# Optimization experiments

Hardware: AMD Instinct MI355X
Metric: run time of the kernel (lower is better)

## Reference

```python
import jax, jax.numpy as jnp
import numpy as np

IN_F = 1024
OUT_F = 1024
GRID = 8
TOKENS = 8192


def setup_inputs() -> dict:
    key = jax.random.key(0)
    k_x, k_w, k_b, k_s = jax.random.split(key, 4)
    x = jax.random.normal(k_x, (TOKENS, IN_F), dtype=jnp.float32)
    # kaiming_uniform_(nonlinearity='linear'): bound = sqrt(3/fan_in)
    bound_w = float(np.sqrt(3.0 / IN_F))
    W = jax.random.uniform(k_w, (OUT_F, IN_F), minval=-bound_w, maxval=bound_w, dtype=jnp.float32)
    # nn.Linear default bias init: U(-1/sqrt(fan_in), 1/sqrt(fan_in))
    bound_b = float(1.0 / np.sqrt(IN_F))
    b = jax.random.uniform(k_b, (OUT_F,), minval=-bound_b, maxval=bound_b, dtype=jnp.float32)
    spline_weight = jax.random.uniform(k_s, (OUT_F, IN_F, GRID), minval=-0.1, maxval=0.1, dtype=jnp.float32)
    grid = jnp.linspace(-3.0, 3.0, GRID, dtype=jnp.float32)
    return {"x": x, "W": W, "b": b, "spline_weight": spline_weight, "grid": grid}


def reference(x, W, b, spline_weight, grid):
    grid_size = spline_weight.shape[-1]
    # base path: Linear(silu(x))
    base = jnp.einsum('ti,oi->to', jax.nn.silu(x), W) + b
    # RBF basis: [tokens, in_features, grid_size]
    denom = 2.0 / (grid_size - 1) + 1e-05
    basis = jnp.exp(-(((x[..., None] - grid) / denom) ** 2))
    spline = jnp.einsum('tig,oig->to', basis, spline_weight)
    return base + spline
```

## Files before the change

kernel.cpp:

```cpp
#include <hip/hip_runtime.h>
#include <hip/hip_bf16.h>

#define IN_F   1024
#define OUT_F  1024
#define TOKENS 8192
#define KTOT   9216
#define KHALF  4608
#define NTILE  72

typedef __attribute__((ext_vector_type(8))) short  bf16x8;
typedef __attribute__((ext_vector_type(4))) float  f32x4;

template<int M> struct ModeT { static constexpr int value = M; };

__device__ __forceinline__ unsigned int f2bf(float f) {
    union { float f; unsigned int u; } v; v.f = f;
    unsigned int r = v.u + 0x7fffu + ((v.u >> 16) & 1u);
    return r >> 16;
}

__device__ __forceinline__ void prep_a_body(int idx, const float* __restrict__ x,
                                            const float* __restrict__ grid,
                                            unsigned short* __restrict__ A)
{
    int t = idx >> 10;
    int i = idx & 1023;
    float xv = x[idx];
    float sil = xv / (1.0f + __expf(-xv));
    A[(size_t)t * KTOT + i] = (unsigned short)f2bf(sil);

    const float invd = 1.0f / (2.0f / 7.0f + 1e-5f);
    unsigned int h[8];
    #pragma unroll
    for (int g = 0; g < 8; ++g) {
        float d = (xv - grid[g]) * invd;
        h[g] = f2bf(__expf(-d * d));
    }
    uint4 pk;
    pk.x = h[0] | (h[1] << 16);
    pk.y = h[2] | (h[3] << 16);
    pk.z = h[4] | (h[5] << 16);
    pk.w = h[6] | (h[7] << 16);
    *reinterpret_cast<uint4*>(&A[(size_t)t * KTOT + IN_F + (size_t)i * 8]) = pk;
}

__device__ __forceinline__ void prep_b_body(int idx, const float* __restrict__ W,
                                            const float* __restrict__ spl,
                                            unsigned short* __restrict__ B)
{
    int o  = idx / (KTOT / 8);
    int c8 = idx - o * (KTOT / 8);
    const float* src = (c8 < IN_F / 8)
        ? (W   + (size_t)o * IN_F     + (size_t)c8 * 8)
        : (spl + (size_t)o * IN_F * 8 + (size_t)(c8 - IN_F / 8) * 8);
    const float4* s4 = reinterpret_cast<const float4*>(src);
    float4 lo = s4[0], hi = s4[1];
    uint4 pk;
    pk.x = f2bf(lo.x) | (f2bf(lo.y) << 16);
    pk.y = f2bf(lo.z) | (f2bf(lo.w) << 16);
    pk.z = f2bf(hi.x) | (f2bf(hi.y) << 16);
    pk.w = f2bf(hi.z) | (f2bf(hi.w) << 16);
    *reinterpret_cast<uint4*>(&B[(size_t)o * KTOT + (size_t)c8 * 8]) = pk;
}

__global__ __launch_bounds__(256)
void prep_fused(const float* __restrict__ x, const float* __restrict__ grid,
                const float* __restrict__ W, const float* __restrict__ spl,
                unsigned short* __restrict__ A, unsigned short* __restrict__ B)
{
    int b = blockIdx.x;
    if (b < (TOKENS * IN_F) / 256)
        prep_a_body(b * 256 + threadIdx.x, x, grid, A);
    else
        prep_b_body((b - (TOKENS * IN_F) / 256) * 256 + threadIdx.x, W, spl, B);
}

__global__ __launch_bounds__(256)
void prep_a_kernel(const float* __restrict__ x, const float* __restrict__ grid,
                   unsigned short* __restrict__ A)
{
    prep_a_body(blockIdx.x * blockDim.x + threadIdx.x, x, grid, A);
}

__global__ __launch_bounds__(256)
void prep_b_kernel(const float* __restrict__ W, const float* __restrict__ spl,
                   unsigned short* __restrict__ B)
{
    prep_b_body(blockIdx.x * blockDim.x + threadIdx.x, W, spl, B);
}

#define GLOAD(src, dst) __builtin_amdgcn_global_load_lds( \
    (const __attribute__((address_space(1))) void*)(src),  \
    (__attribute__((address_space(3))) void*)(dst), 16, 0, 0)
#define SBAR()  __builtin_amdgcn_s_barrier()
#define SCH0()  __builtin_amdgcn_sched_barrier(0)
#define VMC0()  asm volatile("s_waitcnt vmcnt(0)" ::: "memory")

__global__ __launch_bounds__(512, 2)
void gemm_kan2(const unsigned short* __restrict__ A,
               const unsigned short* __restrict__ B,
               float* __restrict__ P, int rows)
{
    __shared__ char lds[131072];

    const int bid  = blockIdx.x;
    const int xcd  = bid & 7;
    const int j    = bid >> 3;
    const int sk   = j & 1;
    const int bn   = (j >> 1) & 3;
    const int bm   = (j >> 3) * 8 + xcd;
    const int tid  = threadIdx.x;
    const int wave = tid >> 6, lane = tid & 63;
    const int wr   = wave >> 2, wc = wave & 3;
    const int fr   = lane & 15, kg = lane >> 4;
    const int sw   = fr & 7;
    const int koff[2] = { (kg ^ sw) * 16, ((4 | kg) ^ sw) * 16 };
    const int k0 = sk * KHALF;

    const int trow = tid >> 3;
    const int ksrc = ((tid & 7) ^ (trow & 7)) * 8;
    const unsigned short* gA = A + (size_t)(bm * 256 + trow) * KTOT + k0 + ksrc;
    const unsigned short* gB = B + (size_t)(bn * 256 + trow) * KTOT + k0 + ksrc;
    const size_t R64 = (size_t)64 * KTOT;

    f32x4 acc[8][4];
    const f32x4 zero = {0.f, 0.f, 0.f, 0.f};
    #pragma unroll
    for (int m = 0; m < 8; ++m)
        #pragma unroll
        for (int n = 0; n < 4; ++n) acc[m][n] = zero;

    {
        char* dA = lds + tid * 16;
        char* dB = lds + 65536 + tid * 16;
        GLOAD(gA,           dA);           GLOAD(gA + R64,     dA + 8192);
        GLOAD(gA + 2 * R64, dA + 16384);   GLOAD(gA + 3 * R64, dA + 24576);
        GLOAD(gB,           dB);           GLOAD(gB + R64,     dB + 8192);
        GLOAD(gB + 2 * R64, dB + 16384);   GLOAD(gB + 3 * R64, dB + 24576);
        gA += 64; gB += 64;
    }
    VMC0(); SBAR(); SCH0();

    const int aOff = (wr * 64 + fr) * 128;
    const int bOff = (wc * 32 + fr) * 128;

    bf16x8 af[4][2], bfLo[2][2], bfHi[2][2];
    int u = 0;

    auto tile = [&](auto mC) {
        constexpr int MODE = decltype(mC)::value;
        char* bufA = lds + (u & 1) * 32768;
        char* bufB = lds + 65536 + (u & 1) * 32768;

        #pragma unroll
        for (int mi = 0; mi < 4; ++mi)
            #pragma unroll
            for (int ks = 0; ks < 2; ++ks)
                af[mi][ks] = *(const bf16x8*)(bufA + aOff + mi * 2048 + koff[ks]);
        #pragma unroll
        for (int ni = 0; ni < 2; ++ni)
            #pragma unroll
            for (int ks = 0; ks < 2; ++ks) {
                bfLo[ni][ks] = *(const bf16x8*)(bufB + bOff + ni * 2048 + koff[ks]);
                bfHi[ni][ks] = *(const bf16x8*)(bufB + bOff + 16384 + ni * 2048 + koff[ks]);
            }

        if constexpr (MODE == 0) {
            char* dA = lds + ((u & 1) ^ 1) * 32768 + tid * 16;
            char* dB = lds + 65536 + ((u & 1) ^ 1) * 32768 + tid * 16;
            GLOAD(gA,           dA);           GLOAD(gA + R64,     dA + 8192);
            GLOAD(gA + 2 * R64, dA + 16384);   GLOAD(gA + 3 * R64, dA + 24576);
            GLOAD(gB,           dB);           GLOAD(gB + R64,     dB + 8192);
            GLOAD(gB + 2 * R64, dB + 16384);   GLOAD(gB + 3 * R64, dB + 24576);
            gA += 64; gB += 64;
        }
        SCH0();

        __builtin_amdgcn_s_setprio(1);
        #pragma unroll
        for (int mi = 0; mi < 4; ++mi)
            #pragma unroll
            for (int ni = 0; ni < 2; ++ni)
                #pragma unroll
                for (int ks = 0; ks < 2; ++ks)
                    acc[mi][ni] = __builtin_amdgcn_mfma_f32_16x16x32_bf16(
                        af[mi][ks], bfLo[ni][ks], acc[mi][ni], 0, 0, 0);
        __builtin_amdgcn_s_setprio(0);

        __builtin_amdgcn_s_setprio(1);
        #pragma unroll
        for (int mi = 0; mi < 4; ++mi)
            #pragma unroll
            for (int ni = 0; ni < 2; ++ni)
                #pragma unroll
                for (int ks = 0; ks < 2; ++ks)
                    acc[mi][2 + ni] = __builtin_amdgcn_mfma_f32_16x16x32_bf16(
                        af[mi][ks], bfHi[ni][ks], acc[mi][2 + ni], 0, 0, 0);
        __builtin_amdgcn_s_setprio(0);

        #pragma unroll
        for (int mi = 0; mi < 4; ++mi)
            #pragma unroll
            for (int ks = 0; ks < 2; ++ks)
                af[mi][ks] = *(const bf16x8*)(bufA + aOff + 16384 + mi * 2048 + koff[ks]);

        __builtin_amdgcn_s_setprio(1);
        #pragma unroll
        for (int mi = 0; mi < 4; ++mi)
            #pragma unroll
            for (int ni = 0; ni < 2; ++ni)
                #pragma unroll
                for (int ks = 0; ks < 2; ++ks)
                    acc[4 + mi][ni] = __builtin_amdgcn_mfma_f32_16x16x32_bf16(
                        af[mi][ks], bfLo[ni][ks], acc[4 + mi][ni], 0, 0, 0);
        __builtin_amdgcn_s_setprio(0);

        __builtin_amdgcn_s_setprio(1);
        #pragma unroll
        for (int mi = 0; mi < 4; ++mi)
            #pragma unroll
            for (int ni = 0; ni < 2; ++ni)
                #pragma unroll
                for (int ks = 0; ks < 2; ++ks)
                    acc[4 + mi][2 + ni] = __builtin_amdgcn_mfma_f32_16x16x32_bf16(
                        af[mi][ks], bfHi[ni][ks], acc[4 + mi][2 + ni], 0, 0, 0);
        __builtin_amdgcn_s_setprio(0);

        SCH0();
        if constexpr (MODE == 0) {
            VMC0();
            SBAR(); SCH0();
        }
    };

    for (u = 0; u < NTILE - 1; ++u) tile(ModeT<0>{});
    tile(ModeT<1>{});

    float* Pp = P + (size_t)sk * rows * OUT_F;
    const size_t orow0 = (size_t)bm * 256 + (size_t)wr * 64;
    const int    ocol0 = bn * 256 + wc * 32;
    #pragma unroll
    for (int n = 0; n < 4; ++n) {
        const int col = ocol0 + (n & 1) * 16 + (n >> 1) * 128 + fr;
        #pragma unroll
        for (int m = 0; m < 8; ++m) {
            const size_t r0 = orow0 + (m & 3) * 16 + (m >> 2) * 128 + kg * 4;
            #pragma unroll
            for (int j2 = 0; j2 < 4; ++j2)
                Pp[(r0 + j2) * OUT_F + col] = acc[m][n][j2];
        }
    }
}

__global__ __launch_bounds__(256)
void reduce_kan(const float* __restrict__ P, const float* __restrict__ bias,
                float* __restrict__ out, int n4, int skStride4)
{
    const float4* p0 = (const float4*)P;
    const float4* p1 = p0 + skStride4;
    const float4* bv = (const float4*)bias;
    float4* o = (float4*)out;
    for (int i = blockIdx.x * blockDim.x + threadIdx.x; i < n4;
         i += gridDim.x * blockDim.x) {
        float4 a = p0[i], b = p1[i], c = bv[i & 255];
        float4 r;
        r.x = a.x + b.x + c.x;  r.y = a.y + b.y + c.y;
        r.z = a.z + b.z + c.z;  r.w = a.w + b.w + c.w;
        o[i] = r;
    }
}

extern "C" void kernel_launch(void* const* d_in, const int* in_sizes, int n_in,
                              void* d_out, int out_size, void* d_ws, size_t ws_size,
                              hipStream_t stream)
{
    const float* x    = (const float*)d_in[0];
    const float* W    = (const float*)d_in[1];
    const float* bias = (const float*)d_in[2];
    const float* spl  = (const float*)d_in[3];
    const float* grid = (const float*)d_in[4];
    float* out = (float*)d_out;

    unsigned short* Bw = (unsigned short*)d_ws;
    unsigned short* Aw = Bw + (size_t)OUT_F * KTOT;

    const size_t bBytes = (size_t)OUT_F * KTOT * 2;
    size_t avail = ws_size > bBytes ? ws_size - bBytes : 0;
    long maxRows = (long)(avail / 26624);
    int chunk = (maxRows >= TOKENS) ? TOKENS : (int)((maxRows / 256) * 256);
    if (chunk < 256) chunk = 256;
    float* Pp = (float*)(Aw + (size_t)chunk * KTOT);

    if (chunk == TOKENS) {
        prep_fused<<<(TOKENS * IN_F) / 256 + (OUT_F * (KTOT / 8)) / 256,
                     256, 0, stream>>>(x, grid, W, spl, Aw, Bw);
        gemm_kan2<<<(TOKENS >> 8) * 8, 512, 0, stream>>>(Aw, Bw, Pp, TOKENS);
        int n4 = TOKENS * 256;
        reduce_kan<<<2048, 256, 0, stream>>>(Pp, bias, out, n4, n4);
    } else {
        prep_b_kernel<<<(OUT_F * (KTOT / 8)) / 256, 256, 0, stream>>>(W, spl, Bw);
        for (int t0 = 0; t0 < TOKENS; t0 += chunk) {
            int rows = (TOKENS - t0 < chunk) ? (TOKENS - t0) : chunk;
            prep_a_kernel<<<(rows * IN_F) / 256, 256, 0, stream>>>(
                x + (size_t)t0 * IN_F, grid, Aw);
            gemm_kan2<<<(rows >> 8) * 8, 512, 0, stream>>>(Aw, Bw, Pp, rows);
            int n4 = rows * 256;
            int rblocks = (n4 + 255) / 256; if (rblocks > 2048) rblocks = 2048;
            reduce_kan<<<rblocks, 256, 0, stream>>>(
                Pp, bias, out + (size_t)t0 * OUT_F, n4, n4);
        }
    }
}
```

Before: 199.1 us.

## Load B fragments directly from global into registers, halve LDS usage

Drops the LDS staging of the B operand: each wave now reads its B fragments straight from global memory into registers and prefetches the next k-step mid-tile, so only A is double-buffered in LDS (64KB instead of 128KB). The A fragments for both halves are loaded up front and the MFMA order is rearranged around the B loads. The XCD-aware block swizzle is also removed in favour of a plain linear block mapping. This frees LDS and cuts LDS traffic, possibly allowing more resident blocks, but B reads lose cross-wave sharing, and the remaining cost is uncoalesced global reads with latency exposed at the per-tile vmcnt(0) wait.

```diff
diff --git a/kernel.cpp b/kernel.cpp
--- a/kernel.cpp
+++ b/kernel.cpp
@@ -101,14 +101,12 @@
                const unsigned short* __restrict__ B,
                float* __restrict__ P, int rows)
 {
-    __shared__ char lds[131072];
+    __shared__ char lds[65536];
 
     const int bid  = blockIdx.x;
-    const int xcd  = bid & 7;
-    const int j    = bid >> 3;
-    const int sk   = j & 1;
-    const int bn   = (j >> 1) & 3;
-    const int bm   = (j >> 3) * 8 + xcd;
+    const int sk   = bid & 1;
+    const int bn   = (bid >> 1) & 3;
+    const int bm   = bid >> 3;
     const int tid  = threadIdx.x;
     const int wave = tid >> 6, lane = tid & 63;
     const int wr   = wave >> 2, wc = wave & 3;
@@ -120,8 +118,12 @@
     const int trow = tid >> 3;
     const int ksrc = ((tid & 7) ^ (trow & 7)) * 8;
     const unsigned short* gA = A + (size_t)(bm * 256 + trow) * KTOT + k0 + ksrc;
-    const unsigned short* gB = B + (size_t)(bn * 256 + trow) * KTOT + k0 + ksrc;
     const size_t R64 = (size_t)64 * KTOT;
+
+    const unsigned short* gB00 = B + (size_t)(bn * 256 + wc * 32 + fr) * KTOT + k0 + kg * 8;
+    const unsigned short* gB01 = gB00 + (size_t)16  * KTOT;
+    const unsigned short* gB10 = gB00 + (size_t)128 * KTOT;
+    const unsigned short* gB11 = gB00 + (size_t)144 * KTOT;
 
     f32x4 acc[8][4];
     const f32x4 zero = {0.f, 0.f, 0.f, 0.f};
@@ -130,49 +132,48 @@
         #pragma unroll
         for (int n = 0; n < 4; ++n) acc[m][n] = zero;
 
+    bf16x8 afLo[4][2], afHi[4][2], bfL[2][2], bfH[2][2];
+
     {
         char* dA = lds + tid * 16;
-        char* dB = lds + 65536 + tid * 16;
         GLOAD(gA,           dA);           GLOAD(gA + R64,     dA + 8192);
         GLOAD(gA + 2 * R64, dA + 16384);   GLOAD(gA + 3 * R64, dA + 24576);
-        GLOAD(gB,           dB);           GLOAD(gB + R64,     dB + 8192);
-        GLOAD(gB + 2 * R64, dB + 16384);   GLOAD(gB + 3 * R64, dB + 24576);
-        gA += 64; gB += 64;
+        gA += 64;
+        #pragma unroll
+        for (int ks = 0; ks < 2; ++ks) {
+            bfL[0][ks] = *(const bf16x8*)(gB00 + ks * 32);
+            bfL[1][ks] = *(const bf16x8*)(gB01 + ks * 32);
+        }
     }
     VMC0(); SBAR(); SCH0();
 
     const int aOff = (wr * 64 + fr) * 128;
-    const int bOff = (wc * 32 + fr) * 128;
-
-    bf16x8 af[4][2], bfLo[2][2], bfHi[2][2];
+
     int u = 0;
 
     auto tile = [&](auto mC) {
         constexpr int MODE = decltype(mC)::value;
         char* bufA = lds + (u & 1) * 32768;
-        char* bufB = lds + 65536 + (u & 1) * 32768;
-
-        #pragma unroll
-        for (int mi = 0; mi < 4; ++mi)
-            #pragma unroll
-            for (int ks = 0; ks < 2; ++ks)
-                af[mi][ks] = *(const bf16x8*)(bufA + aOff + mi * 2048 + koff[ks]);
-        #pragma unroll
-        for (int ni = 0; ni < 2; ++ni)
+
+        #pragma unroll
+        for (int mi = 0; mi < 4; ++mi)
             #pragma unroll
             for (int ks = 0; ks < 2; ++ks) {
-                bfLo[ni][ks] = *(const bf16x8*)(bufB + bOff + ni * 2048 + koff[ks]);
-                bfHi[ni][ks] = *(const bf16x8*)(bufB + bOff + 16384 + ni * 2048 + koff[ks]);
+                afLo[mi][ks] = *(const bf16x8*)(bufA + aOff + mi * 2048 + koff[ks]);
+                afHi[mi][ks] = *(const bf16x8*)(bufA + aOff + 16384 + mi * 2048 + koff[ks]);
             }
+
+        #pragma unroll
+        for (int ks = 0; ks < 2; ++ks) {
+            bfH[0][ks] = *(const bf16x8*)(gB10 + ks * 32);
+            bfH[1][ks] = *(const bf16x8*)(gB11 + ks * 32);
+        }
 
         if constexpr (MODE == 0) {
             char* dA = lds + ((u & 1) ^ 1) * 32768 + tid * 16;
-            char* dB = lds + 65536 + ((u & 1) ^ 1) * 32768 + tid * 16;
             GLOAD(gA,           dA);           GLOAD(gA + R64,     dA + 8192);
             GLOAD(gA + 2 * R64, dA + 16384);   GLOAD(gA + 3 * R64, dA + 24576);
-            GLOAD(gB,           dB);           GLOAD(gB + R64,     dB + 8192);
-            GLOAD(gB + 2 * R64, dB + 16384);   GLOAD(gB + 3 * R64, dB + 24576);
-            gA += 64; gB += 64;
+            gA += 64;
         }
         SCH0();
 
@@ -184,8 +185,27 @@
                 #pragma unroll
                 for (int ks = 0; ks < 2; ++ks)
                     acc[mi][ni] = __builtin_amdgcn_mfma_f32_16x16x32_bf16(
-                        af[mi][ks], bfLo[ni][ks], acc[mi][ni], 0, 0, 0);
+                        afLo[mi][ks], bfL[ni][ks], acc[mi][ni], 0, 0, 0);
         __builtin_amdgcn_s_setprio(0);
+
+        __builtin_amdgcn_s_setprio(1);
+        #pragma unroll
+        for (int mi = 0; mi < 4; ++mi)
+            #pragma unroll
+            for (int ni = 0; ni < 2; ++ni)
+                #pragma unroll
+                for (int ks = 0; ks < 2; ++ks)
+                    acc[4 + mi][ni] = __builtin_amdgcn_mfma_f32_16x16x32_bf16(
+                        afHi[mi][ks], bfL[ni][ks], acc[4 + mi][ni], 0, 0, 0);
+        __builtin_amdgcn_s_setprio(0);
+
+        if constexpr (MODE == 0) {
+            #pragma unroll
+            for (int ks = 0; ks < 2; ++ks) {
+                bfL[0][ks] = *(const bf16x8*)(gB00 + 64 + ks * 32);
+                bfL[1][ks] = *(const bf16x8*)(gB01 + 64 + ks * 32);
+            }
+        }
 
         __builtin_amdgcn_s_setprio(1);
         #pragma unroll
@@ -195,24 +215,7 @@
                 #pragma unroll
                 for (int ks = 0; ks < 2; ++ks)
                     acc[mi][2 + ni] = __builtin_amdgcn_mfma_f32_16x16x32_bf16(
-                        af[mi][ks], bfHi[ni][ks], acc[mi][2 + ni], 0, 0, 0);
-        __builtin_amdgcn_s_setprio(0);
-
-        #pragma unroll
-        for (int mi = 0; mi < 4; ++mi)
-            #pragma unroll
-            for (int ks = 0; ks < 2; ++ks)
-                af[mi][ks] = *(const bf16x8*)(bufA + aOff + 16384 + mi * 2048 + koff[ks]);
-
-        __builtin_amdgcn_s_setprio(1);
-        #pragma unroll
-        for (int mi = 0; mi < 4; ++mi)
-            #pragma unroll
-            for (int ni = 0; ni < 2; ++ni)
-                #pragma unroll
-                for (int ks = 0; ks < 2; ++ks)
-                    acc[4 + mi][ni] = __builtin_amdgcn_mfma_f32_16x16x32_bf16(
-                        af[mi][ks], bfLo[ni][ks], acc[4 + mi][ni], 0, 0, 0);
+                        afLo[mi][ks], bfH[ni][ks], acc[mi][2 + ni], 0, 0, 0);
         __builtin_amdgcn_s_setprio(0);
 
         __builtin_amdgcn_s_setprio(1);
@@ -223,13 +226,14 @@
                 #pragma unroll
                 for (int ks = 0; ks < 2; ++ks)
                     acc[4 + mi][2 + ni] = __builtin_amdgcn_mfma_f32_16x16x32_bf16(
-                        af[mi][ks], bfHi[ni][ks], acc[4 + mi][2 + ni], 0, 0, 0);
+                        afHi[mi][ks], bfH[ni][ks], acc[4 + mi][2 + ni], 0, 0, 0);
         __builtin_amdgcn_s_setprio(0);
 
         SCH0();
         if constexpr (MODE == 0) {
             VMC0();
             SBAR(); SCH0();
+            gB00 += 64; gB01 += 64; gB10 += 64; gB11 += 64;
         }
     };
 
```

Measured after the change: 262.6 us. 1.32x slower.

## Deepen GEMM pipeline with two tiles in flight and register-level fragment prefetch

Applied to the files above, without the earlier changes.

Restructures the bf16 MFMA main loop so two K-tiles of global-to-LDS loads are in flight and the next half-tile's LDS fragments are loaded into registers while the current MFMAs run. A single barrier per tile now separates consumption from refill, and the loop is split into steady, penultimate and last phases. The block-index mapping also drops the XCD-aware swizzle in favour of a plain linear decode. This raises register pressure from the doubled fragment sets and may change L2 locality across XCDs.

```diff
diff --git a/kernel.cpp b/kernel.cpp
--- a/kernel.cpp
+++ b/kernel.cpp
@@ -94,7 +94,9 @@
     (__attribute__((address_space(3))) void*)(dst), 16, 0, 0)
 #define SBAR()  __builtin_amdgcn_s_barrier()
 #define SCH0()  __builtin_amdgcn_sched_barrier(0)
+#define LGKM0() asm volatile("s_waitcnt lgkmcnt(0)" ::: "memory")
 #define VMC0()  asm volatile("s_waitcnt vmcnt(0)" ::: "memory")
+#define VMCNT_(n) asm volatile("s_waitcnt vmcnt(" #n ")" ::: "memory")
 
 __global__ __launch_bounds__(512, 2)
 void gemm_kan2(const unsigned short* __restrict__ A,
@@ -104,17 +106,16 @@
     __shared__ char lds[131072];
 
     const int bid  = blockIdx.x;
-    const int xcd  = bid & 7;
-    const int j    = bid >> 3;
-    const int sk   = j & 1;
-    const int bn   = (j >> 1) & 3;
-    const int bm   = (j >> 3) * 8 + xcd;
+    const int sk   = bid & 1;
+    const int bn   = (bid >> 1) & 3;
+    const int bm   = bid >> 3;
     const int tid  = threadIdx.x;
     const int wave = tid >> 6, lane = tid & 63;
     const int wr   = wave >> 2, wc = wave & 3;
     const int fr   = lane & 15, kg = lane >> 4;
     const int sw   = fr & 7;
-    const int koff[2] = { (kg ^ sw) * 16, ((4 | kg) ^ sw) * 16 };
+    const int koff0 = (kg ^ sw) * 16;
+    const int koff1 = ((4 | kg) ^ sw) * 16;
     const int k0 = sk * KHALF;
 
     const int trow = tid >> 3;
@@ -138,103 +139,84 @@
         GLOAD(gB,           dB);           GLOAD(gB + R64,     dB + 8192);
         GLOAD(gB + 2 * R64, dB + 16384);   GLOAD(gB + 3 * R64, dB + 24576);
         gA += 64; gB += 64;
-    }
-    VMC0(); SBAR(); SCH0();
+        dA += 32768; dB += 32768;
+        GLOAD(gA,           dA);           GLOAD(gA + R64,     dA + 8192);
+        GLOAD(gA + 2 * R64, dA + 16384);   GLOAD(gA + 3 * R64, dA + 24576);
+        GLOAD(gB,           dB);           GLOAD(gB + R64,     dB + 8192);
+        GLOAD(gB + 2 * R64, dB + 16384);   GLOAD(gB + 3 * R64, dB + 24576);
+        gA += 64; gB += 64;
+    }
+    VMCNT_(8); SBAR(); SCH0();
 
     const int aOff = (wr * 64 + fr) * 128;
-    const int bOff = (wc * 32 + fr) * 128;
-
-    bf16x8 af[4][2], bfLo[2][2], bfHi[2][2];
+    const int bOff = 65536 + (wc * 32 + fr) * 128;
+
+    bf16x8 af0[8], bf0[4], af1[8], bf1[4];
+
+    #pragma unroll
+    for (int j = 0; j < 8; ++j)
+        af0[j] = *(const bf16x8*)(lds + aOff + (j & 3) * 2048 + (j >> 2) * 16384 + koff0);
+    #pragma unroll
+    for (int n = 0; n < 4; ++n)
+        bf0[n] = *(const bf16x8*)(lds + bOff + (n & 1) * 2048 + (n >> 1) * 16384 + koff0);
+
     int u = 0;
 
     auto tile = [&](auto mC) {
         constexpr int MODE = decltype(mC)::value;
-        char* bufA = lds + (u & 1) * 32768;
-        char* bufB = lds + 65536 + (u & 1) * 32768;
-
-        #pragma unroll
-        for (int mi = 0; mi < 4; ++mi)
-            #pragma unroll
-            for (int ks = 0; ks < 2; ++ks)
-                af[mi][ks] = *(const bf16x8*)(bufA + aOff + mi * 2048 + koff[ks]);
-        #pragma unroll
-        for (int ni = 0; ni < 2; ++ni)
-            #pragma unroll
-            for (int ks = 0; ks < 2; ++ks) {
-                bfLo[ni][ks] = *(const bf16x8*)(bufB + bOff + ni * 2048 + koff[ks]);
-                bfHi[ni][ks] = *(const bf16x8*)(bufB + bOff + 16384 + ni * 2048 + koff[ks]);
-            }
-
+        char* bufAc = lds + (u & 1) * 32768;
+        char* bufBc = bufAc + 65536;
+        char* bufAn = lds + ((u & 1) ^ 1) * 32768;
+        char* bufBn = bufAn + 65536;
+
+        #pragma unroll
+        for (int j = 0; j < 8; ++j)
+            af1[j] = *(const bf16x8*)(bufAc + aOff + (j & 3) * 2048 + (j >> 2) * 16384 + koff1);
+        #pragma unroll
+        for (int n = 0; n < 4; ++n)
+            bf1[n] = *(const bf16x8*)(bufBc + bOff - 65536 + (n & 1) * 2048 + (n >> 1) * 16384 + koff1);
+        __builtin_amdgcn_s_setprio(1);
+        #pragma unroll
+        for (int j = 0; j < 8; ++j)
+            #pragma unroll
+            for (int n = 0; n < 4; ++n)
+                acc[j][n] = __builtin_amdgcn_mfma_f32_16x16x32_bf16(
+                    af0[j], bf0[n], acc[j][n], 0, 0, 0);
+        __builtin_amdgcn_s_setprio(0);
+
+        SCH0(); LGKM0(); VMC0(); SBAR(); SCH0();
+
+        if constexpr (MODE <= 1) {
+            #pragma unroll
+            for (int j = 0; j < 8; ++j)
+                af0[j] = *(const bf16x8*)(bufAn + aOff + (j & 3) * 2048 + (j >> 2) * 16384 + koff0);
+            #pragma unroll
+            for (int n = 0; n < 4; ++n)
+                bf0[n] = *(const bf16x8*)(bufBn + bOff - 65536 + (n & 1) * 2048 + (n >> 1) * 16384 + koff0);
+        }
         if constexpr (MODE == 0) {
-            char* dA = lds + ((u & 1) ^ 1) * 32768 + tid * 16;
-            char* dB = lds + 65536 + ((u & 1) ^ 1) * 32768 + tid * 16;
+            char* dA = bufAc + tid * 16;
+            char* dB = bufBc + tid * 16;
             GLOAD(gA,           dA);           GLOAD(gA + R64,     dA + 8192);
             GLOAD(gA + 2 * R64, dA + 16384);   GLOAD(gA + 3 * R64, dA + 24576);
             GLOAD(gB,           dB);           GLOAD(gB + R64,     dB + 8192);
             GLOAD(gB + 2 * R64, dB + 16384);   GLOAD(gB + 3 * R64, dB + 24576);
             gA += 64; gB += 64;
         }
-        SCH0();
-
         __builtin_amdgcn_s_setprio(1);
         #pragma unroll
-        for (int mi = 0; mi < 4; ++mi)
-            #pragma unroll
-            for (int ni = 0; ni < 2; ++ni)
-                #pragma unroll
-                for (int ks = 0; ks < 2; ++ks)
-                    acc[mi][ni] = __builtin_amdgcn_mfma_f32_16x16x32_bf16(
-                        af[mi][ks], bfLo[ni][ks], acc[mi][ni], 0, 0, 0);
+        for (int j = 0; j < 8; ++j)
+            #pragma unroll
+            for (int n = 0; n < 4; ++n)
+                acc[j][n] = __builtin_amdgcn_mfma_f32_16x16x32_bf16(
+                    af1[j], bf1[n], acc[j][n], 0, 0, 0);
         __builtin_amdgcn_s_setprio(0);
-
-        __builtin_amdgcn_s_setprio(1);
-        #pragma unroll
-        for (int mi = 0; mi < 4; ++mi)
-            #pragma unroll
-            for (int ni = 0; ni < 2; ++ni)
-                #pragma unroll
-                for (int ks = 0; ks < 2; ++ks)
-                    acc[mi][2 + ni] = __builtin_amdgcn_mfma_f32_16x16x32_bf16(
-                        af[mi][ks], bfHi[ni][ks], acc[mi][2 + ni], 0, 0, 0);
-        __builtin_amdgcn_s_setprio(0);
-
-        #pragma unroll
-        for (int mi = 0; mi < 4; ++mi)
-            #pragma unroll
-            for (int ks = 0; ks < 2; ++ks)
-                af[mi][ks] = *(const bf16x8*)(bufA + aOff + 16384 + mi * 2048 + koff[ks]);
-
-        __builtin_amdgcn_s_setprio(1);
-        #pragma unroll
-        for (int mi = 0; mi < 4; ++mi)
-            #pragma unroll
-            for (int ni = 0; ni < 2; ++ni)
-                #pragma unroll
-                for (int ks = 0; ks < 2; ++ks)
-                    acc[4 + mi][ni] = __builtin_amdgcn_mfma_f32_16x16x32_bf16(
-                        af[mi][ks], bfLo[ni][ks], acc[4 + mi][ni], 0, 0, 0);
-        __builtin_amdgcn_s_setprio(0);
-
-        __builtin_amdgcn_s_setprio(1);
-        #pragma unroll
-        for (int mi = 0; mi < 4; ++mi)
-            #pragma unroll
-            for (int ni = 0; ni < 2; ++ni)
-                #pragma unroll
-                for (int ks = 0; ks < 2; ++ks)
-                    acc[4 + mi][2 + ni] = __builtin_amdgcn_mfma_f32_16x16x32_bf16(
-                        af[mi][ks], bfHi[ni][ks], acc[4 + mi][2 + ni], 0, 0, 0);
-        __builtin_amdgcn_s_setprio(0);
-
-        SCH0();
-        if constexpr (MODE == 0) {
-            VMC0();
-            SBAR(); SCH0();
-        }
     };
 
-    for (u = 0; u < NTILE - 1; ++u) tile(ModeT<0>{});
+    for (u = 0; u < NTILE - 2; ++u) tile(ModeT<0>{});
     tile(ModeT<1>{});
+    ++u;
+    tile(ModeT<2>{});
 
     float* Pp = P + (size_t)sk * rows * OUT_F;
     const size_t orow0 = (size_t)bm * 256 + (size_t)wr * 64;
```

Result: faster. 193.4 us (-2.9%).

## Store split-K partials as bf16 and simplify block-to-tile mapping

Applied to the files above, without the earlier changes.

The GEMM now writes its two split-K partial results in bf16 instead of fp32, and the reduce kernel reads bf16 pairs, converts them to float and adds the bias. This halves the partial-buffer write and read traffic (about 64 MB down to 32 MB). The block index mapping also drops the XCD-aware remapping in favour of a plain linear layout, which changes L2 locality across the chiplets. Rounding the partials to bf16 adds error to the output.

```diff
diff --git a/kernel.cpp b/kernel.cpp
--- a/kernel.cpp
+++ b/kernel.cpp
@@ -9,6 +9,7 @@
 #define NTILE  72
 
 typedef __attribute__((ext_vector_type(8))) short  bf16x8;
+typedef __attribute__((ext_vector_type(8))) unsigned short ushortx8;
 typedef __attribute__((ext_vector_type(4))) float  f32x4;
 
 template<int M> struct ModeT { static constexpr int value = M; };
@@ -17,6 +18,11 @@
     union { float f; unsigned int u; } v; v.f = f;
     unsigned int r = v.u + 0x7fffu + ((v.u >> 16) & 1u);
     return r >> 16;
+}
+
+__device__ __forceinline__ float bf2f(unsigned short h) {
+    union { unsigned int u; float f; } v; v.u = ((unsigned int)h) << 16;
+    return v.f;
 }
 
 __device__ __forceinline__ void prep_a_body(int idx, const float* __restrict__ x,
@@ -99,16 +105,14 @@
 __global__ __launch_bounds__(512, 2)
 void gemm_kan2(const unsigned short* __restrict__ A,
                const unsigned short* __restrict__ B,
-               float* __restrict__ P, int rows)
+               unsigned short* __restrict__ P, int rows)
 {
     __shared__ char lds[131072];
 
     const int bid  = blockIdx.x;
-    const int xcd  = bid & 7;
-    const int j    = bid >> 3;
-    const int sk   = j & 1;
-    const int bn   = (j >> 1) & 3;
-    const int bm   = (j >> 3) * 8 + xcd;
+    const int sk   = bid & 1;
+    const int bn   = (bid >> 1) & 3;
+    const int bm   = bid >> 3;
     const int tid  = threadIdx.x;
     const int wave = tid >> 6, lane = tid & 63;
     const int wr   = wave >> 2, wc = wave & 3;
@@ -236,7 +240,7 @@
     for (u = 0; u < NTILE - 1; ++u) tile(ModeT<0>{});
     tile(ModeT<1>{});
 
-    float* Pp = P + (size_t)sk * rows * OUT_F;
+    unsigned short* Pp = P + (size_t)sk * rows * OUT_F;
     const size_t orow0 = (size_t)bm * 256 + (size_t)wr * 64;
     const int    ocol0 = bn * 256 + wc * 32;
     #pragma unroll
@@ -247,26 +251,35 @@
             const size_t r0 = orow0 + (m & 3) * 16 + (m >> 2) * 128 + kg * 4;
             #pragma unroll
             for (int j2 = 0; j2 < 4; ++j2)
-                Pp[(r0 + j2) * OUT_F + col] = acc[m][n][j2];
+                Pp[(r0 + j2) * OUT_F + col] = (unsigned short)f2bf(acc[m][n][j2]);
         }
     }
 }
 
 __global__ __launch_bounds__(256)
-void reduce_kan(const float* __restrict__ P, const float* __restrict__ bias,
-                float* __restrict__ out, int n4, int skStride4)
-{
-    const float4* p0 = (const float4*)P;
-    const float4* p1 = p0 + skStride4;
+void reduce_kan(const unsigned short* __restrict__ P,
+                const float* __restrict__ bias,
+                float* __restrict__ out, int n8, int skStride8)
+{
+    const ushortx8* p0 = (const ushortx8*)P;
+    const ushortx8* p1 = p0 + skStride8;
     const float4* bv = (const float4*)bias;
     float4* o = (float4*)out;
-    for (int i = blockIdx.x * blockDim.x + threadIdx.x; i < n4;
+    for (int i = blockIdx.x * blockDim.x + threadIdx.x; i < n8;
          i += gridDim.x * blockDim.x) {
-        float4 a = p0[i], b = p1[i], c = bv[i & 255];
-        float4 r;
-        r.x = a.x + b.x + c.x;  r.y = a.y + b.y + c.y;
-        r.z = a.z + b.z + c.z;  r.w = a.w + b.w + c.w;
-        o[i] = r;
+        ushortx8 a = p0[i], b = p1[i];
+        float4 c0 = bv[(i & 127) * 2], c1 = bv[(i & 127) * 2 + 1];
+        float4 r0, r1;
+        r0.x = bf2f(a[0]) + bf2f(b[0]) + c0.x;
+        r0.y = bf2f(a[1]) + bf2f(b[1]) + c0.y;
+        r0.z = bf2f(a[2]) + bf2f(b[2]) + c0.z;
+        r0.w = bf2f(a[3]) + bf2f(b[3]) + c0.w;
+        r1.x = bf2f(a[4]) + bf2f(b[4]) + c1.x;
+        r1.y = bf2f(a[5]) + bf2f(b[5]) + c1.y;
+        r1.z = bf2f(a[6]) + bf2f(b[6]) + c1.z;
+        r1.w = bf2f(a[7]) + bf2f(b[7]) + c1.w;
+        o[i * 2]     = r0;
+        o[i * 2 + 1] = r1;
     }
 }
 
@@ -286,17 +299,17 @@
 
     const size_t bBytes = (size_t)OUT_F * KTOT * 2;
     size_t avail = ws_size > bBytes ? ws_size - bBytes : 0;
-    long maxRows = (long)(avail / 26624);
+    long maxRows = (long)(avail / 22528);
     int chunk = (maxRows >= TOKENS) ? TOKENS : (int)((maxRows / 256) * 256);
     if (chunk < 256) chunk = 256;
-    float* Pp = (float*)(Aw + (size_t)chunk * KTOT);
+    unsigned short* Pp = Aw + (size_t)chunk * KTOT;
 
     if (chunk == TOKENS) {
         prep_fused<<<(TOKENS * IN_F) / 256 + (OUT_F * (KTOT / 8)) / 256,
                      256, 0, stream>>>(x, grid, W, spl, Aw, Bw);
         gemm_kan2<<<(TOKENS >> 8) * 8, 512, 0, stream>>>(Aw, Bw, Pp, TOKENS);
-        int n4 = TOKENS * 256;
-        reduce_kan<<<2048, 256, 0, stream>>>(Pp, bias, out, n4, n4);
+        int n8 = TOKENS * 128;
+        reduce_kan<<<2048, 256, 0, stream>>>(Pp, bias, out, n8, n8);
     } else {
         prep_b_kernel<<<(OUT_F * (KTOT / 8)) / 256, 256, 0, stream>>>(W, spl, Bw);
         for (int t0 = 0; t0 < TOKENS; t0 += chunk) {
@@ -304,10 +317,10 @@
             prep_a_kernel<<<(rows * IN_F) / 256, 256, 0, stream>>>(
                 x + (size_t)t0 * IN_F, grid, Aw);
             gemm_kan2<<<(rows >> 8) * 8, 512, 0, stream>>>(Aw, Bw, Pp, rows);
-            int n4 = rows * 256;
-            int rblocks = (n4 + 255) / 256; if (rblocks > 2048) rblocks = 2048;
+            int n8 = rows * 128;
+            int rblocks = (n8 + 255) / 256; if (rblocks > 2048) rblocks = 2048;
             reduce_kan<<<rblocks, 256, 0, stream>>>(
-                Pp, bias, out + (size_t)t0 * OUT_F, n4, n4);
+                Pp, bias, out + (size_t)t0 * OUT_F, n8, n8);
         }
     }
 }
```

After: 180.4 us. -9.4%, faster.
